# Optimization experiments

Hardware: AMD Instinct MI355X
Metric: run time of the kernel (lower is better)

## Reference

```python
import jax, jax.numpy as jnp
import numpy as np


def _l2norm(x, axis):
    return x / jnp.maximum(jnp.linalg.norm(x, axis=axis, keepdims=True), 1e-12)


def _conv1x1(x, w, b=None):
    # x: [B,C,H,W], w: [O,C]
    y = jnp.einsum('bchw,oc->bohw', x, w)
    if b is not None:
        y = y + b[None, :, None, None]
    return y


def _layernorm(x, g, b, eps=1e-5):
    m = x.mean(-1, keepdims=True)
    v = x.var(-1, keepdims=True)
    return (x - m) / jnp.sqrt(v + eps) * g + b


def _bn_eval(x, g, b, eps=1e-5):
    # eval-mode BatchNorm2d with running_mean=0, running_var=1
    return x * (g / jnp.sqrt(1.0 + eps))[None, :, None, None] + b[None, :, None, None]


def setup_inputs() -> dict:
    key = jax.random.key(0)
    ks = jax.random.split(key, 24)
    B, C, H, W, M, P, DS = 4, 128, 128, 128, 5, 4, 4
    s = 0.05

    def n(k, shape, scale=s):
        return jax.random.normal(k, shape, jnp.float32) * scale

    m_items = _l2norm(jax.random.uniform(ks[2], (M, C), jnp.float32), axis=1)
    return {
        'Structure': jax.random.normal(ks[0], (B, C, H, W), jnp.float32),
        'query': jax.random.normal(ks[1], (B, C, H, W), jnp.float32),
        'm_items': m_items,
        'mod_w': n(ks[3], (M * C, C)), 'mod_b': jnp.zeros((M * C,), jnp.float32),
        'conv1_w': n(ks[4], (C // 2, M * C)), 'conv1_b': jnp.zeros((C // 2,), jnp.float32),
        'conv2_w': n(ks[5], (C // 2, C)), 'conv2_b': jnp.zeros((C // 2,), jnp.float32),
        'pe_w': n(ks[6], (C, C, P, P)), 'pe_b': jnp.zeros((C,), jnp.float32),
        'pe_g': jnp.ones((C,), jnp.float32), 'pe_beta': jnp.zeros((C,), jnp.float32),
        'exp_w': n(ks[7], (C, DS * C)),
        'fin_g': jnp.ones((C // DS,), jnp.float32), 'fin_b': jnp.zeros((C // DS,), jnp.float32),
        'up_w': n(ks[8], (C, C // DS)), 'up_b': jnp.zeros((C,), jnp.float32),
        'wf_w2': jnp.ones((2,), jnp.float32),
        'wf_pre_w': n(ks[9], (C, C)),
        'wf_post_w': n(ks[10], (C, C, 3, 3)),
        'wf_bn_g': jnp.ones((C,), jnp.float32),
        'wf_bn_b': jnp.full((C,), 1e-4, jnp.float32),
    }


def reference(Structure, query, m_items, mod_w, mod_b, conv1_w, conv1_b,
              conv2_w, conv2_b, pe_w, pe_b, pe_g, pe_beta, exp_w, fin_g,
              fin_b, up_w, up_b, wf_w2, wf_pre_w, wf_post_w, wf_bn_g, wf_bn_b):
    M, C = m_items.shape
    B, _, H, W = Structure.shape
    P = pe_w.shape[-1]
    DS = exp_w.shape[1] // C

    # ---- read() ----
    s = _l2norm(Structure, axis=1)                            # F.normalize over channels
    mod = jax.nn.sigmoid(_conv1x1(s, mod_w, mod_b))           # [B, M*C, H, W]
    mod = mod.reshape(B, M, C, H, W)
    M0 = m_items[None, :, :, None, None] * mod                # broadcast memory slots, [B,M,C,H,W]
    c1w = conv1_w.reshape(-1, M, C)
    M0c = jnp.einsum('bmchw,omc->bohw', M0, c1w) + conv1_b[None, :, None, None]
    Sc = _conv1x1(s, conv2_w, conv2_b)
    Sn = jnp.concatenate([M0c, Sc], axis=1)                   # [B, C, H, W]

    # PatchEmbed2D: conv k=P, stride=P, then NHWC LayerNorm
    xs = Sn.reshape(B, C, H // P, P, W // P, P)
    f = jnp.einsum('bchpwq,ocpq->bhwo', xs, pe_w) + pe_b      # [B, H/P, W/P, C]
    f = _layernorm(f, pe_g, pe_beta)

    # HierarchicalVSSBlock: identity passthrough (definition not in repo snippet)

    # Final_PatchExpand2D: Linear(dim -> DS*dim), pixel-shuffle by DS, LN(dim//DS)
    h, w = H // P, W // P
    c = C // DS
    fe = f @ exp_w                                            # [B,h,w,DS*C]
    fe = fe.reshape(B, h, w, DS, DS, c).transpose(0, 1, 3, 2, 4, 5)
    fe = fe.reshape(B, h * DS, w * DS, c)
    fe = _layernorm(fe, fin_g, fin_b)
    fe = fe.transpose(0, 3, 1, 2)                             # [B, C//DS, H, W]
    M1 = _conv1x1(fe, up_w, up_b)                             # [B, C, H, W]

    # WF fusion
    ww = jax.nn.relu(wf_w2)
    fwt = ww / (ww.sum() + 1e-8)
    x = fwt[0] * _conv1x1(query, wf_pre_w) + fwt[1] * M1
    y = jax.lax.conv_general_dilated(x, wf_post_w, (1, 1), ((1, 1), (1, 1)),
                                     dimension_numbers=('NCHW', 'OIHW', 'NCHW'))
    y = _bn_eval(y, wf_bn_g, wf_bn_b)
    return jnp.clip(y, 0.0, 6.0)                              # ReLU6
```

## Files before the change

kernel.cpp:

```cpp
#include <hip/hip_runtime.h>

typedef unsigned short u16;
typedef unsigned int u32;
typedef __attribute__((ext_vector_type(8))) short bf16x8;
typedef __attribute__((ext_vector_type(4))) float f32x4;

__device__ __forceinline__ float b2f(u16 h) {
  union { u32 u; float f; } v; v.u = ((u32)h) << 16; return v.f;
}
__device__ __forceinline__ u16 f2b(float x) {
  union { float f; u32 u; } v; v.f = x;
  u32 u = v.u;
  return (u16)((u + 0x7FFFu + ((u >> 16) & 1u)) >> 16);
}
__device__ __forceinline__ void up2(u32 u, float& lo, float& hi) {
  union { u32 x; float f; } a, b;
  a.x = u << 16; b.x = u & 0xFFFF0000u;
  lo = a.f; hi = b.f;
}
__device__ __forceinline__ u32 pk2(float lo, float hi) {
  return (u32)f2b(lo) | ((u32)f2b(hi) << 16);
}

__global__ __launch_bounds__(256) void k_prep(
    const float* __restrict__ mod_w, const float* __restrict__ conv1_w,
    const float* __restrict__ m_items, const float* __restrict__ conv2_w,
    const float* __restrict__ wf_pre_w, const float* __restrict__ wf_post_w,
    const float* __restrict__ wf_bn_g, const float* __restrict__ pe_w,
    const float* __restrict__ exp_w, const float* __restrict__ up_w,
    u16* __restrict__ wcomb, u16* __restrict__ c2F,
    u16* __restrict__ wpreF, u16* __restrict__ wpk, u16* __restrict__ pewB,
    u16* __restrict__ expB, u16* __restrict__ upF)
{
  int idx = blockIdx.x * 256 + threadIdx.x;
  if (idx < 122880) {
    int chunk = idx / 12288, r = idx % 12288;
    float val;
    if (r < 8192) {
      int e = r & 7, lane = (r >> 3) & 63, fr = r >> 9;
      int ks = fr >> 2, ct = fr & 3;
      int chan = chunk * 64 + ct * 16 + (lane & 15);
      int c = ks * 32 + ((lane >> 4) << 3) + e;
      val = mod_w[chan * 128 + c];
    } else {
      int r2 = r - 8192;
      int e = r2 & 7, lane = (r2 >> 3) & 63, fr = r2 >> 9;
      int kt = fr >> 2, nt = fr & 3;
      int o = nt * 16 + (lane & 15);
      int k = chunk * 64 + kt * 32 + ((lane >> 4) << 3) + e;
      val = conv1_w[o * 640 + k] * m_items[k];
    }
    wcomb[idx] = f2b(val);
  } else if (idx < 131072) {
    int i = idx - 122880;
    c2F[i] = f2b(conv2_w[i]);
  } else if (idx < 147456) {
    int i = idx - 131072;
    wpreF[i] = f2b(wf_pre_w[i]);
  } else if (idx < 294912) {
    int i2 = idx - 147456;
    int e = i2 & 7;
    int r = i2 >> 3;
    int lane = r & 63; r >>= 6;
    int n = r & 7; r >>= 3;
    int tap = r % 9, ks = r / 9;
    int o = (n << 4) + (lane & 15);
    int ic = (ks << 5) + ((lane >> 4) << 3) + e;
    int dy = tap / 3, dx = tap % 3;
    float scale = wf_bn_g[o] * rsqrtf(1.f + 1e-5f);
    wpk[i2] = f2b(wf_post_w[((o * 128 + ic) * 3 + dy) * 3 + dx] * scale);
  } else if (idx < 557056) {
    int i = idx - 294912;
    int e = i & 7;
    int r = i >> 3;
    int lane = r & 63; r >>= 6;
    int n = r & 7;
    int gks = r >> 3;
    int o = (n << 4) + (lane & 15);
    int kp = (gks << 5) + ((lane >> 4) << 3) + e;
    int p = kp >> 9, c = (kp >> 2) & 127, q = kp & 3;
    int k = c * 16 + p * 4 + q;
    pewB[i] = f2b(pe_w[o * 2048 + k]);
  } else if (idx < 622592) {
    int i = idx - 557056;
    int j = i >> 7, c = i & 127;
    expB[i] = f2b(exp_w[c * 512 + j]);
  } else if (idx < 626688) {
    int i = idx - 622592;
    upF[i] = f2b(up_w[i]);
  }
}

__global__ __launch_bounds__(256) void k_read(
    const float* __restrict__ S, const u16* __restrict__ wcomb,
    const u16* __restrict__ c2F,
    const float* __restrict__ mod_b,
    const float* __restrict__ conv1_b, const float* __restrict__ conv2_b,
    u16* __restrict__ Snp)
{
  __shared__ u16 xs[16384];
  __shared__ u16 modL[8192];
  __shared__ u16 wbuf[12288];
  __shared__ float rn[128];
  __shared__ float ps[2][128];
  __shared__ float mbL[640];

  const int t = threadIdx.x;
  const int b = blockIdx.x >> 7;
  const int y = blockIdx.x & 127;
  const int hw0 = y << 7;

  {
    const int pix = t & 127, ch = t >> 7;
    const float* Sp = S + ((size_t)b << 21) + (size_t)hw0 + pix;
    float ss = 0.f;
    #pragma unroll
    for (int c0 = 0; c0 < 64; c0 += 8) {
      float v[8]; u32 pkv[4];
      #pragma unroll
      for (int j = 0; j < 8; ++j) {
        v[j] = Sp[(size_t)(ch * 64 + c0 + j) << 14];
        ss += v[j] * v[j];
      }
      #pragma unroll
      for (int j = 0; j < 4; ++j) pkv[j] = pk2(v[2 * j], v[2 * j + 1]);
      int e = pix * 256 + (ch * 64 + c0) * 2;
      e ^= (pix & 7) << 4;
      *(uint4*)((char*)xs + e) = *(const uint4*)pkv;
    }
    ps[ch][pix] = ss;
  }
  for (int i = t; i < 640; i += 256) mbL[i] = mod_b[i];
  __syncthreads();
  if (t < 128) rn[t] = 1.f / fmaxf(sqrtf(ps[0][t] + ps[1][t]), 1e-12f);

  const int w = t >> 6, l = t & 63;
  const int g = l >> 4, cl = l & 15;
  const int pxw = w << 5;
  const int swz = (cl & 7) << 4;

  __syncthreads();
  float rncol[2] = { rn[pxw + cl], rn[pxw + 16 + cl] };

  f32x4 acc2[2][4];
  #pragma unroll
  for (int pt = 0; pt < 2; ++pt)
    #pragma unroll
    for (int nt = 0; nt < 4; ++nt) acc2[pt][nt] = (f32x4){0.f, 0.f, 0.f, 0.f};

  for (int i = 0; i < 10; ++i) {
    const int n0 = i << 6;
    __syncthreads();
    {
      const u16* wsrc = wcomb + i * 12288;
      #pragma unroll
      for (int j = 0; j < 6; ++j) {
        uint4 v = *(const uint4*)(wsrc + (((j << 8) + t) << 3));
        *(uint4*)((char*)wbuf + (((j << 8) + t) << 4)) = v;
      }
    }
    __syncthreads();

    f32x4 acc1[4][2];
    #pragma unroll
    for (int ct = 0; ct < 4; ++ct)
      #pragma unroll
      for (int pt = 0; pt < 2; ++pt) acc1[ct][pt] = (f32x4){0.f, 0.f, 0.f, 0.f};
    #pragma unroll
    for (int ks = 0; ks < 4; ++ks) {
      bf16x8 xf[2];
      #pragma unroll
      for (int pt = 0; pt < 2; ++pt) {
        int pix = pxw + (pt << 4) + cl;
        int e = (pix * 256 + ks * 64 + g * 16) ^ swz;
        xf[pt] = *(const bf16x8*)((const char*)xs + e);
      }
      #pragma unroll
      for (int ct = 0; ct < 4; ++ct) {
        bf16x8 wf = *(const bf16x8*)((const char*)wbuf + (((ks << 2) + ct) << 10) + (l << 4));
        acc1[ct][0] = __builtin_amdgcn_mfma_f32_16x16x32_bf16(wf, xf[0], acc1[ct][0], 0, 0, 0);
        acc1[ct][1] = __builtin_amdgcn_mfma_f32_16x16x32_bf16(wf, xf[1], acc1[ct][1], 0, 0, 0);
      }
    }

    #pragma unroll
    for (int pt = 0; pt < 2; ++pt) {
      int pix = pxw + (pt << 4) + cl;
      float rv = rncol[pt];
      #pragma unroll
      for (int ct = 0; ct < 4; ++ct) {
        float4 mb4 = *(const float4*)&mbL[n0 + (ct << 4) + (g << 2)];
        f32x4 a = acc1[ct][pt];
        float m[4];
        #pragma unroll
        for (int r = 0; r < 4; ++r) {
          float z = a[r] * rv + ((const float*)&mb4)[r];
          m[r] = __builtin_amdgcn_rcpf(1.f + __expf(-z));
        }
        u32 lo, hi;
        asm("v_cvt_pk_bf16_f32 %0, %1, %2" : "=v"(lo) : "v"(m[0]), "v"(m[1]));
        asm("v_cvt_pk_bf16_f32 %0, %1, %2" : "=v"(hi) : "v"(m[2]), "v"(m[3]));
        int e = (pix * 128 + ct * 32 + g * 8) ^ swz;
        uint2 st = { lo, hi };
        *(uint2*)((char*)modL + e) = st;
      }
    }

    #pragma unroll
    for (int kt = 0; kt < 2; ++kt) {
      bf16x8 af[2];
      #pragma unroll
      for (int pt = 0; pt < 2; ++pt) {
        int pix = pxw + (pt << 4) + cl;
        int e = (pix * 128 + kt * 64 + g * 16) ^ swz;
        af[pt] = *(const bf16x8*)((const char*)modL + e);
      }
      #pragma unroll
      for (int nt = 0; nt < 4; ++nt) {
        bf16x8 bfr = *(const bf16x8*)((const char*)wbuf + 16384 + (((kt << 2) + nt) << 10) + (l << 4));
        acc2[0][nt] = __builtin_amdgcn_mfma_f32_16x16x32_bf16(af[0], bfr, acc2[0][nt], 0, 0, 0);
        acc2[1][nt] = __builtin_amdgcn_mfma_f32_16x16x32_bf16(af[1], bfr, acc2[1][nt], 0, 0, 0);
      }
    }
  }

  f32x4 acc3[2][4];
  #pragma unroll
  for (int pt = 0; pt < 2; ++pt)
    #pragma unroll
    for (int nt = 0; nt < 4; ++nt) acc3[pt][nt] = (f32x4){0.f, 0.f, 0.f, 0.f};
  #pragma unroll
  for (int ks = 0; ks < 4; ++ks) {
    bf16x8 af[2];
    #pragma unroll
    for (int pt = 0; pt < 2; ++pt) {
      int pix = pxw + (pt << 4) + cl;
      int e = (pix * 256 + ks * 64 + g * 16) ^ swz;
      af[pt] = *(const bf16x8*)((const char*)xs + e);
    }
    #pragma unroll
    for (int nt = 0; nt < 4; ++nt) {
      bf16x8 bfr = *(const bf16x8*)&c2F[(size_t)((nt << 4) + cl) * 128 + ks * 32 + g * 8];
      acc3[0][nt] = __builtin_amdgcn_mfma_f32_16x16x32_bf16(af[0], bfr, acc3[0][nt], 0, 0, 0);
      acc3[1][nt] = __builtin_amdgcn_mfma_f32_16x16x32_bf16(af[1], bfr, acc3[1][nt], 0, 0, 0);
    }
  }

  const int pgrp = (b << 5) + (y >> 2);
  u16* Srow = Snp + ((size_t)pgrp << 16) + ((y & 3) << 9);
  #pragma unroll
  for (int pt = 0; pt < 2; ++pt) {
    int pixr = pxw + (pt << 4) + (g << 2);
    float4 rn4 = *(const float4*)&rn[pixr];
    int pw = pixr >> 2;
    #pragma unroll
    for (int nt = 0; nt < 4; ++nt) {
      int c = (nt << 4) + cl;
      float b1 = conv1_b[c];
      f32x4 a2 = acc2[pt][nt];
      uint2 s0 = { pk2(a2[0] + b1, a2[1] + b1), pk2(a2[2] + b1, a2[3] + b1) };
      *(uint2*)&Srow[((size_t)pw << 11) + (c << 2)] = s0;
      float b2 = conv2_b[c];
      f32x4 a3 = acc3[pt][nt];
      uint2 s1v = { pk2(a3[0] * rn4.x + b2, a3[1] * rn4.y + b2),
                    pk2(a3[2] * rn4.z + b2, a3[3] * rn4.w + b2) };
      *(uint2*)&Srow[((size_t)pw << 11) + ((c + 64) << 2)] = s1v;
    }
  }
}

__global__ __launch_bounds__(512) void k_pe_ex(
    const u16* __restrict__ Snp, const u16* __restrict__ pewB,
    const float* __restrict__ pe_b, const float* __restrict__ pe_g,
    const float* __restrict__ pe_beta,
    const u16* __restrict__ expB,
    const float* __restrict__ fin_g, const float* __restrict__ fin_b,
    const u16* __restrict__ upF, const float* __restrict__ up_b,
    u16* __restrict__ M1b)
{
  __shared__ u16 As[8192];
  __shared__ float fln[16][132];
  __shared__ u16 fb[2048];
  __shared__ u16 feL[8192];
  __shared__ u16 feL2[8192];
  __shared__ float lng[32], lnb[32];
  const int t = threadIdx.x, bx = blockIdx.x;
  const int w = t >> 6, l = t & 63;
  const int g = l >> 4, cl = l & 15;
  const size_t gbase = (size_t)bx << 15;
  const int pg0 = bx << 4;

  if (t < 32) { lng[t] = fin_g[t]; lnb[t] = fin_b[t]; }

  f32x4 acc = (f32x4){0.f, 0.f, 0.f, 0.f};

  for (int chunk = 0; chunk < 4; ++chunk) {
    __syncthreads();
    #pragma unroll
    for (int it = 0; it < 2; ++it) {
      int e8 = ((it << 9) + t) << 3;
      int pl = e8 >> 9, kk = e8 & 511;
      uint4 v = *(const uint4*)&Snp[gbase + ((size_t)pl << 11) + (chunk << 9) + kk];
      int e = (((pl << 9) + kk) << 1) ^ ((pl & 7) << 4);
      *(uint4*)((char*)As + e) = v;
    }
    __syncthreads();
    for (int ks = 0; ks < 16; ++ks) {
      int kk = (ks << 5) + (g << 3);
      int e = (((cl << 9) + kk) << 1) ^ ((cl & 7) << 4);
      bf16x8 A = *(const bf16x8*)((const char*)As + e);
      int gks = (chunk << 4) + ks;
      bf16x8 B = *(const bf16x8*)&pewB[(size_t)((((gks << 3) + w) << 6) + l) << 3];
      acc = __builtin_amdgcn_mfma_f32_16x16x32_bf16(A, B, acc, 0, 0, 0);
    }
  }

  {
    int o = (w << 4) + cl;
    float pb = pe_b[o];
    #pragma unroll
    for (int r = 0; r < 4; ++r)
      fln[(g << 2) + r][o] = acc[r] + pb;
  }
  __syncthreads();

  if (t < 128) {
    int patch = t >> 3, sub = t & 7;
    float4 v0 = *(const float4*)&fln[patch][(sub << 4) + 0];
    float4 v1 = *(const float4*)&fln[patch][(sub << 4) + 4];
    float4 v2 = *(const float4*)&fln[patch][(sub << 4) + 8];
    float4 v3 = *(const float4*)&fln[patch][(sub << 4) + 12];
    float s1 = v0.x + v0.y + v0.z + v0.w + v1.x + v1.y + v1.z + v1.w
             + v2.x + v2.y + v2.z + v2.w + v3.x + v3.y + v3.z + v3.w;
    float s2 = v0.x*v0.x + v0.y*v0.y + v0.z*v0.z + v0.w*v0.w
             + v1.x*v1.x + v1.y*v1.y + v1.z*v1.z + v1.w*v1.w
             + v2.x*v2.x + v2.y*v2.y + v2.z*v2.z + v2.w*v2.w
             + v3.x*v3.x + v3.y*v3.y + v3.z*v3.z + v3.w*v3.w;
    s1 += __shfl_xor(s1, 1); s2 += __shfl_xor(s2, 1);
    s1 += __shfl_xor(s1, 2); s2 += __shfl_xor(s2, 2);
    s1 += __shfl_xor(s1, 4); s2 += __shfl_xor(s2, 4);
    float m = s1 * (1.f / 128.f);
    float var = s2 * (1.f / 128.f) - m * m;
    float rs = rsqrtf(var + 1e-5f);
    int o0 = sub << 4;
    #pragma unroll
    for (int i = 0; i < 4; ++i) {
      float4 vv = (i == 0) ? v0 : (i == 1) ? v1 : (i == 2) ? v2 : v3;
      float4 gv = *(const float4*)&pe_g[o0 + (i << 2)];
      float4 bv = *(const float4*)&pe_beta[o0 + (i << 2)];
      uint2 st = { pk2((vv.x - m) * rs * gv.x + bv.x, (vv.y - m) * rs * gv.y + bv.y),
                   pk2((vv.z - m) * rs * gv.z + bv.z, (vv.w - m) * rs * gv.w + bv.w) };
      int c = o0 + (i << 2);
      int e = (patch * 256 + c * 2) ^ ((patch & 7) << 4);
      *(uint2*)((char*)fb + e) = st;
    }
  }
  __syncthreads();

  f32x4 acc1[4];
  #pragma unroll
  for (int jj = 0; jj < 4; ++jj) acc1[jj] = (f32x4){0.f, 0.f, 0.f, 0.f};
  #pragma unroll
  for (int ks = 0; ks < 4; ++ks) {
    int e = (cl * 256 + ks * 64 + g * 16) ^ ((cl & 7) << 4);
    bf16x8 ff = *(const bf16x8*)((const char*)fb + e);
    #pragma unroll
    for (int jj = 0; jj < 4; ++jj) {
      int jt = (w << 2) + jj;
      bf16x8 wf = *(const bf16x8*)&expB[(size_t)((jt << 4) + cl) * 128 + ks * 32 + g * 8];
      acc1[jj] = __builtin_amdgcn_mfma_f32_16x16x32_bf16(wf, ff, acc1[jj], 0, 0, 0);
    }
  }
  #pragma unroll
  for (int jj = 0; jj < 4; ++jj) {
    int j0 = (((w << 2) + jj) << 4) + (g << 2);
    f32x4 a = acc1[jj];
    uint2 st = { pk2(a[0], a[1]), pk2(a[2], a[3]) };
    int e = (cl * 1024 + j0 * 2) ^ ((cl & 7) << 3);
    *(uint2*)((char*)feL + e) = st;
  }
  __syncthreads();

  if (t < 256) {
    int patch = t >> 4, sub = t & 15;
    int rot = t & 15;
    int baseR = patch * 1024 + sub * 64;
    int xr = (patch & 7) << 3;
    float vals[32];
    float s1 = 0.f, s2 = 0.f;
    #pragma unroll
    for (int wd = 0; wd < 16; ++wd) {
      int ww = (wd + rot) & 15;
      u32 u = *(const u32*)((const char*)feL + ((baseR + ww * 4) ^ xr));
      float lo, hi; up2(u, lo, hi);
      vals[wd * 2] = lo; vals[wd * 2 + 1] = hi;
      s1 += lo + hi; s2 += lo * lo + hi * hi;
    }
    float m = s1 * (1.f / 32.f);
    float var = s2 * (1.f / 32.f) - m * m;
    float rs = rsqrtf(var + 1e-5f);
    int baseW = t * 64;
    int xw = (t & 3) << 4;
    #pragma unroll
    for (int wd = 0; wd < 16; ++wd) {
      int ww = (wd + rot) & 15;
      float lo = (vals[wd * 2]     - m) * rs * lng[ww * 2]     + lnb[ww * 2];
      float hi = (vals[wd * 2 + 1] - m) * rs * lng[ww * 2 + 1] + lnb[ww * 2 + 1];
      *(u32*)((char*)feL2 + ((baseW + ww * 4) ^ xw)) = pk2(lo, hi);
    }
  }
  __syncthreads();

  #pragma unroll
  for (int mt4 = 0; mt4 < 2; ++mt4) {
    int pixl = (((w << 1) + mt4) << 4) + cl;
    int e = (pixl * 64 + g * 16) ^ ((pixl & 3) << 4);
    bf16x8 fef = *(const bf16x8*)((const char*)feL2 + e);
    int pglob = pg0 + (pixl >> 4);
    int sub = pixl & 15;
    int bb = pglob >> 10, ph = (pglob >> 5) & 31, pw = pglob & 31;
    int yy = (ph << 2) + (sub >> 2), xx = (pw << 2) + (sub & 3);
    size_t mbase = ((size_t)(((bb << 7) + yy) << 7) + xx) << 7;
    f32x4 accu[8];
    #pragma unroll
    for (int nt = 0; nt < 8; ++nt) {
      bf16x8 wfu = *(const bf16x8*)&upF[((nt << 4) + cl) * 32 + g * 8];
      accu[nt] = __builtin_amdgcn_mfma_f32_16x16x32_bf16(
          wfu, fef, (f32x4){0.f, 0.f, 0.f, 0.f}, 0, 0, 0);
    }
    #pragma unroll
    for (int nt = 0; nt < 8; ++nt) {
      int o0 = (nt << 4) + (g << 2);
      float4 ub4 = *(const float4*)&up_b[o0];
      f32x4 a = accu[nt];
      uint2 st = { pk2(a[0] + ub4.x, a[1] + ub4.y),
                   pk2(a[2] + ub4.z, a[3] + ub4.w) };
      *(uint2*)&M1b[mbase + o0] = st;
    }
  }
}

__global__ __launch_bounds__(256) void k_wf(
    const float* __restrict__ Q, const u16* __restrict__ wpreF,
    const u16* __restrict__ M1b, const float* __restrict__ w2,
    u16* __restrict__ Xn)
{
  __shared__ u16 qs[16384];
  const int t = threadIdx.x;
  const int b = blockIdx.x >> 7;
  const int hw0 = (blockIdx.x & 127) << 7;

  {
    const int pix = t & 127, ch = t >> 7;
    const float* Qp = Q + ((size_t)b << 21) + (size_t)hw0 + pix;
    #pragma unroll
    for (int c0 = 0; c0 < 64; c0 += 8) {
      float v[8]; u32 pkv[4];
      #pragma unroll
      for (int j = 0; j < 8; ++j)
        v[j] = Qp[(size_t)(ch * 64 + c0 + j) << 14];
      #pragma unroll
      for (int j = 0; j < 4; ++j) pkv[j] = pk2(v[2 * j], v[2 * j + 1]);
      int e = pix * 256 + (ch * 64 + c0) * 2;
      e ^= (pix & 7) << 4;
      *(uint4*)((char*)qs + e) = *(const uint4*)pkv;
    }
  }
  __syncthreads();

  const int w = t >> 6, l = t & 63;
  const int g = l >> 4, cl = l & 15;
  const int pxw = w << 5;
  const int swz = (cl & 7) << 4;

  f32x4 acc[2][8];
  #pragma unroll
  for (int pt = 0; pt < 2; ++pt)
    #pragma unroll
    for (int ot = 0; ot < 8; ++ot) acc[pt][ot] = (f32x4){0.f, 0.f, 0.f, 0.f};

  #pragma unroll
  for (int ks = 0; ks < 4; ++ks) {
    bf16x8 qf[2];
    #pragma unroll
    for (int pt = 0; pt < 2; ++pt) {
      int pix = pxw + (pt << 4) + cl;
      int e = (pix * 256 + ks * 64 + g * 16) ^ swz;
      qf[pt] = *(const bf16x8*)((const char*)qs + e);
    }
    #pragma unroll
    for (int ot = 0; ot < 8; ++ot) {
      bf16x8 wf = *(const bf16x8*)&wpreF[(size_t)((ot << 4) + cl) * 128 + ks * 32 + g * 8];
      acc[0][ot] = __builtin_amdgcn_mfma_f32_16x16x32_bf16(wf, qf[0], acc[0][ot], 0, 0, 0);
      acc[1][ot] = __builtin_amdgcn_mfma_f32_16x16x32_bf16(wf, qf[1], acc[1][ot], 0, 0, 0);
    }
  }

  float a0 = fmaxf(w2[0], 0.f), a1 = fmaxf(w2[1], 0.f);
  float inv = 1.f / (a0 + a1 + 1e-8f);
  float f0 = a0 * inv, f1 = a1 * inv;

  #pragma unroll
  for (int pt = 0; pt < 2; ++pt) {
    int pix = pxw + (pt << 4) + cl;
    size_t pbase = ((size_t)((b << 14) + hw0 + pix)) << 7;
    #pragma unroll
    for (int ot = 0; ot < 8; ++ot) {
      int o0 = (ot << 4) + (g << 2);
      uint2 mv = *(const uint2*)&M1b[pbase + o0];
      float m0, m1, m2, m3;
      up2(mv.x, m0, m1); up2(mv.y, m2, m3);
      f32x4 a = acc[pt][ot];
      uint2 st = { pk2(f0 * a[0] + f1 * m0, f0 * a[1] + f1 * m1),
                   pk2(f0 * a[2] + f1 * m2, f0 * a[3] + f1 * m3) };
      *(uint2*)&Xn[pbase + o0] = st;
    }
  }
}

__global__ __launch_bounds__(256) void k_conv3(
    const u16* __restrict__ Xn, const u16* __restrict__ wpk,
    const float* __restrict__ bnb, float* __restrict__ out)
{
  __shared__ u16 it[12800];
  __shared__ u16 wb[24576];
  const int t = threadIdx.x, bx = blockIdx.x;
  const int b = bx >> 8, rem = bx & 255;
  const int ty8 = (rem >> 4) << 3, tx8 = (rem & 15) << 3;
  const int y0 = ty8 - 1, x0 = tx8 - 1;

  for (int idx = t; idx < 1600; idx += 256) {
    int ri = idx >> 4, cc = idx & 15;
    int gy = y0 + ri / 10, gx = x0 + ri % 10;
    uint4 v = {0u, 0u, 0u, 0u};
    if (gy >= 0 && gy < 128 && gx >= 0 && gx < 128)
      v = *(const uint4*)&Xn[(((size_t)(b << 14) + (gy << 7) + gx) << 7) + (cc << 3)];
    int e = (ri << 7) + (cc << 3);
    e ^= (ri & 7) << 3;
    *(uint4*)&it[e] = v;
  }

  const int w = t >> 6, l = t & 63;
  const int g = l >> 4, cl = l & 15;

  f32x4 acc[4][2];
  #pragma unroll
  for (int m = 0; m < 4; ++m)
    #pragma unroll
    for (int nn = 0; nn < 2; ++nn)
      acc[m][nn] = (f32x4){0.f, 0.f, 0.f, 0.f};

  int ri0[4];
  #pragma unroll
  for (int m = 0; m < 4; ++m) {
    int p = (m << 4) + cl;
    ri0[m] = (p >> 3) * 10 + (p & 7);
  }

  #pragma unroll
  for (int p = 0; p < 6; ++p) {
    __syncthreads();
    {
      const u16* wsrc = wpk + p * 24576;
      #pragma unroll
      for (int j = 0; j < 12; ++j) {
        uint4 v = *(const uint4*)(wsrc + (((j << 8) + t) << 3));
        *(uint4*)((char*)wb + (((j << 8) + t) << 4)) = v;
      }
    }
    __syncthreads();

    #pragma unroll
    for (int tl = 0; tl < 6; ++tl) {
      const int q = p * 6 + tl;
      const int ks = q / 9, tap = q % 9;
      const int dy = tap / 3, dx = tap % 3;
      bf16x8 A[4];
      #pragma unroll
      for (int m = 0; m < 4; ++m) {
        int ri = ri0[m] + dy * 10 + dx;
        int e = (ri << 7) + (ks << 5) + (g << 3);
        e ^= (ri & 7) << 3;
        A[m] = *(const bf16x8*)&it[e];
      }
      #pragma unroll
      for (int nn = 0; nn < 2; ++nn) {
        int n = (w << 1) + nn;
        bf16x8 B = *(const bf16x8*)((const char*)wb + (((tl << 3) + n) << 10) + (l << 4));
        #pragma unroll
        for (int m = 0; m < 4; ++m)
          acc[m][nn] = __builtin_amdgcn_mfma_f32_16x16x32_bf16(A[m], B, acc[m][nn], 0, 0, 0);
      }
    }
  }

  #pragma unroll
  for (int m = 0; m < 4; ++m) {
    int p = (m << 4) + (g << 2);
    int py = p >> 3, px = p & 7;
    #pragma unroll
    for (int nn = 0; nn < 2; ++nn) {
      int n = (w << 1) + nn;
      int o = (n << 4) + cl;
      float bb = bnb[o];
      f32x4 a = acc[m][nn];
      float4 v = { fminf(fmaxf(a[0] + bb, 0.f), 6.f),
                   fminf(fmaxf(a[1] + bb, 0.f), 6.f),
                   fminf(fmaxf(a[2] + bb, 0.f), 6.f),
                   fminf(fmaxf(a[3] + bb, 0.f), 6.f) };
      *(float4*)&out[((size_t)((b << 7) + o) << 14) + ((ty8 + py) << 7) + tx8 + px] = v;
    }
  }
}

extern "C" void kernel_launch(void* const* d_in, const int* in_sizes, int n_in,
                              void* d_out, int out_size, void* d_ws, size_t ws_size,
                              hipStream_t stream) {
  const float* Structure = (const float*)d_in[0];
  const float* query     = (const float*)d_in[1];
  const float* m_items   = (const float*)d_in[2];
  const float* mod_w     = (const float*)d_in[3];
  const float* mod_b     = (const float*)d_in[4];
  const float* conv1_w   = (const float*)d_in[5];
  const float* conv1_b   = (const float*)d_in[6];
  const float* conv2_w   = (const float*)d_in[7];
  const float* conv2_b   = (const float*)d_in[8];
  const float* pe_w      = (const float*)d_in[9];
  const float* pe_b      = (const float*)d_in[10];
  const float* pe_g      = (const float*)d_in[11];
  const float* pe_beta   = (const float*)d_in[12];
  const float* exp_w     = (const float*)d_in[13];
  const float* fin_g     = (const float*)d_in[14];
  const float* fin_b     = (const float*)d_in[15];
  const float* up_w      = (const float*)d_in[16];
  const float* up_b      = (const float*)d_in[17];
  const float* wf_w2     = (const float*)d_in[18];
  const float* wf_pre_w  = (const float*)d_in[19];
  const float* wf_post_w = (const float*)d_in[20];
  const float* wf_bn_g   = (const float*)d_in[21];
  const float* wf_bn_b   = (const float*)d_in[22];

  char* ws = (char*)d_ws;
  u16*   Snp = (u16*)(ws + 0);
  u16*   expB = (u16*)(ws + 34603008);
  u16*   upF  = (u16*)(ws + 34734080);
  u16*   M1b = (u16*)(ws + 35651584);
  u16*   Xn  = (u16*)(ws + 0);
  u16* wcomb = (u16*)(ws + 69206016);
  u16* c2F   = (u16*)(ws + 69451776);
  u16* wpreF = (u16*)(ws + 69468160);
  u16* wpk   = (u16*)(ws + 69500928);
  u16* pewB  = (u16*)(ws + 69795840);

  k_prep<<<2448, 256, 0, stream>>>(mod_w, conv1_w, m_items, conv2_w, wf_pre_w,
                                   wf_post_w, wf_bn_g, pe_w, exp_w, up_w,
                                   wcomb, c2F, wpreF, wpk, pewB, expB, upF);
  k_read<<<512, 256, 0, stream>>>(Structure, wcomb, c2F, mod_b,
                                  conv1_b, conv2_b, Snp);
  k_pe_ex<<<256, 512, 0, stream>>>(Snp, pewB, pe_b, pe_g, pe_beta,
                                   expB, fin_g, fin_b, upF, up_b, M1b);
  k_wf<<<512, 256, 0, stream>>>(query, wpreF, M1b, wf_w2, Xn);
  k_conv3<<<1024, 256, 0, stream>>>(Xn, wpk, wf_bn_b, (float*)d_out);
}
```

Measured before the change: 124.4 us.

## Fuse WF pre-conv and blend into 3x3 conv kernel with halo recompute

```diff
diff --git a/kernel.cpp b/kernel.cpp
--- a/kernel.cpp
+++ b/kernel.cpp
@@ -440,108 +440,82 @@
   }
 }
 
-__global__ __launch_bounds__(256) void k_wf(
+__global__ __launch_bounds__(256) void k_conv3(
     const float* __restrict__ Q, const u16* __restrict__ wpreF,
     const u16* __restrict__ M1b, const float* __restrict__ w2,
-    u16* __restrict__ Xn)
-{
-  __shared__ u16 qs[16384];
-  const int t = threadIdx.x;
-  const int b = blockIdx.x >> 7;
-  const int hw0 = (blockIdx.x & 127) << 7;
-
-  {
-    const int pix = t & 127, ch = t >> 7;
-    const float* Qp = Q + ((size_t)b << 21) + (size_t)hw0 + pix;
-    #pragma unroll
-    for (int c0 = 0; c0 < 64; c0 += 8) {
-      float v[8]; u32 pkv[4];
-      #pragma unroll
-      for (int j = 0; j < 8; ++j)
-        v[j] = Qp[(size_t)(ch * 64 + c0 + j) << 14];
-      #pragma unroll
-      for (int j = 0; j < 4; ++j) pkv[j] = pk2(v[2 * j], v[2 * j + 1]);
-      int e = pix * 256 + (ch * 64 + c0) * 2;
-      e ^= (pix & 7) << 4;
-      *(uint4*)((char*)qs + e) = *(const uint4*)pkv;
-    }
-  }
-  __syncthreads();
-
-  const int w = t >> 6, l = t & 63;
-  const int g = l >> 4, cl = l & 15;
-  const int pxw = w << 5;
-  const int swz = (cl & 7) << 4;
-
-  f32x4 acc[2][8];
-  #pragma unroll
-  for (int pt = 0; pt < 2; ++pt)
-    #pragma unroll
-    for (int ot = 0; ot < 8; ++ot) acc[pt][ot] = (f32x4){0.f, 0.f, 0.f, 0.f};
-
-  #pragma unroll
-  for (int ks = 0; ks < 4; ++ks) {
-    bf16x8 qf[2];
-    #pragma unroll
-    for (int pt = 0; pt < 2; ++pt) {
-      int pix = pxw + (pt << 4) + cl;
-      int e = (pix * 256 + ks * 64 + g * 16) ^ swz;
-      qf[pt] = *(const bf16x8*)((const char*)qs + e);
-    }
-    #pragma unroll
-    for (int ot = 0; ot < 8; ++ot) {
-      bf16x8 wf = *(const bf16x8*)&wpreF[(size_t)((ot << 4) + cl) * 128 + ks * 32 + g * 8];
-      acc[0][ot] = __builtin_amdgcn_mfma_f32_16x16x32_bf16(wf, qf[0], acc[0][ot], 0, 0, 0);
-      acc[1][ot] = __builtin_amdgcn_mfma_f32_16x16x32_bf16(wf, qf[1], acc[1][ot], 0, 0, 0);
-    }
-  }
-
-  float a0 = fmaxf(w2[0], 0.f), a1 = fmaxf(w2[1], 0.f);
-  float inv = 1.f / (a0 + a1 + 1e-8f);
-  float f0 = a0 * inv, f1 = a1 * inv;
-
-  #pragma unroll
-  for (int pt = 0; pt < 2; ++pt) {
-    int pix = pxw + (pt << 4) + cl;
-    size_t pbase = ((size_t)((b << 14) + hw0 + pix)) << 7;
-    #pragma unroll
-    for (int ot = 0; ot < 8; ++ot) {
-      int o0 = (ot << 4) + (g << 2);
-      uint2 mv = *(const uint2*)&M1b[pbase + o0];
-      float m0, m1, m2, m3;
-      up2(mv.x, m0, m1); up2(mv.y, m2, m3);
-      f32x4 a = acc[pt][ot];
-      uint2 st = { pk2(f0 * a[0] + f1 * m0, f0 * a[1] + f1 * m1),
-                   pk2(f0 * a[2] + f1 * m2, f0 * a[3] + f1 * m3) };
-      *(uint2*)&Xn[pbase + o0] = st;
-    }
-  }
-}
-
-__global__ __launch_bounds__(256) void k_conv3(
-    const u16* __restrict__ Xn, const u16* __restrict__ wpk,
-    const float* __restrict__ bnb, float* __restrict__ out)
+    const u16* __restrict__ wpk, const float* __restrict__ bnb,
+    float* __restrict__ out)
 {
   __shared__ u16 it[12800];
-  __shared__ u16 wb[24576];
+  __shared__ u16 pool[24576];
+  u16* qs = pool;
+  u16* wb = pool;
   const int t = threadIdx.x, bx = blockIdx.x;
   const int b = bx >> 8, rem = bx & 255;
   const int ty8 = (rem >> 4) << 3, tx8 = (rem & 15) << 3;
   const int y0 = ty8 - 1, x0 = tx8 - 1;
 
+  float a0 = fmaxf(w2[0], 0.f), a1 = fmaxf(w2[1], 0.f);
+  float inv = 1.f / (a0 + a1 + 1e-8f);
+  float f0 = a0 * inv, f1 = a1 * inv;
+
   for (int idx = t; idx < 1600; idx += 256) {
     int ri = idx >> 4, cc = idx & 15;
     int gy = y0 + ri / 10, gx = x0 + ri % 10;
-    uint4 v = {0u, 0u, 0u, 0u};
-    if (gy >= 0 && gy < 128 && gx >= 0 && gx < 128)
-      v = *(const uint4*)&Xn[(((size_t)(b << 14) + (gy << 7) + gx) << 7) + (cc << 3)];
+    u32 pkv[4] = {0u, 0u, 0u, 0u};
+    if (gy >= 0 && gy < 128 && gx >= 0 && gx < 128) {
+      const float* Qp = Q + ((((size_t)(b << 7) + (cc << 3)) << 7) + gy) * 128 + gx;
+      float v[8];
+      #pragma unroll
+      for (int j = 0; j < 8; ++j) v[j] = Qp[(size_t)j << 14];
+      #pragma unroll
+      for (int j = 0; j < 4; ++j) pkv[j] = pk2(v[2 * j], v[2 * j + 1]);
+    }
     int e = (ri << 7) + (cc << 3);
     e ^= (ri & 7) << 3;
-    *(uint4*)&it[e] = v;
-  }
+    *(uint4*)&qs[e] = *(const uint4*)pkv;
+  }
+  __syncthreads();
 
   const int w = t >> 6, l = t & 63;
   const int g = l >> 4, cl = l & 15;
+
+  #pragma unroll
+  for (int m = 0; m < 7; ++m) {
+    int pix = (m << 4) + cl;
+    int ri = (pix < 100) ? pix : 99;
+    bf16x8 qf[4];
+    #pragma unroll
+    for (int ks = 0; ks < 4; ++ks) {
+      int e = (ri << 7) + (ks << 5) + (g << 3);
+      e ^= (ri & 7) << 3;
+      qf[ks] = *(const bf16x8*)&qs[e];
+    }
+    #pragma unroll
+    for (int ot2 = 0; ot2 < 2; ++ot2) {
+      int ot = (w << 1) + ot2;
+      f32x4 accq = (f32x4){0.f, 0.f, 0.f, 0.f};
+      #pragma unroll
+      for (int ks = 0; ks < 4; ++ks) {
+        bf16x8 wf = *(const bf16x8*)&wpreF[(size_t)((ot << 4) + cl) * 128 + ks * 32 + g * 8];
+        accq = __builtin_amdgcn_mfma_f32_16x16x32_bf16(wf, qf[ks], accq, 0, 0, 0);
+      }
+      if (pix < 100) {
+        int gy = y0 + pix / 10, gx = x0 + pix % 10;
+        int o0 = (ot << 4) + (g << 2);
+        uint2 mv = {0u, 0u};
+        if (gy >= 0 && gy < 128 && gx >= 0 && gx < 128)
+          mv = *(const uint2*)&M1b[((((size_t)(b << 7) + gy) << 7) + gx) * 128 + o0];
+        float m0, m1, m2, m3;
+        up2(mv.x, m0, m1); up2(mv.y, m2, m3);
+        uint2 st = { pk2(f0 * accq[0] + f1 * m0, f0 * accq[1] + f1 * m1),
+                     pk2(f0 * accq[2] + f1 * m2, f0 * accq[3] + f1 * m3) };
+        int e = (ri << 7) + o0;
+        e ^= (ri & 7) << 3;
+        *(uint2*)&it[e] = st;
+      }
+    }
+  }
 
   f32x4 acc[4][2];
   #pragma unroll
@@ -645,7 +619,6 @@
   u16*   expB = (u16*)(ws + 34603008);
   u16*   upF  = (u16*)(ws + 34734080);
   u16*   M1b = (u16*)(ws + 35651584);
-  u16*   Xn  = (u16*)(ws + 0);
   u16* wcomb = (u16*)(ws + 69206016);
   u16* c2F   = (u16*)(ws + 69451776);
   u16* wpreF = (u16*)(ws + 69468160);
@@ -659,6 +632,6 @@
                                   conv1_b, conv2_b, Snp);
   k_pe_ex<<<256, 512, 0, stream>>>(Snp, pewB, pe_b, pe_g, pe_beta,
                                    expB, fin_g, fin_b, upF, up_b, M1b);
-  k_wf<<<512, 256, 0, stream>>>(query, wpreF, M1b, wf_w2, Xn);
-  k_conv3<<<1024, 256, 0, stream>>>(Xn, wpk, wf_bn_b, (float*)d_out);
-}
+  k_conv3<<<1024, 256, 0, stream>>>(query, wpreF, M1b, wf_w2, wpk, wf_bn_b,
+                                    (float*)d_out);
+}
```

After: 150.6 us. +21.1%, slower.
